# Performance work log

Hardware: AMD Instinct MI355X
Metric: run time of the kernel (lower is better)

Reference implementation:

```python
import jax, jax.numpy as jnp
import numpy as np

B, L, D, H, DFF, WS = 8, 16384, 256, 8, 1024, 32
HD = D // H
NW = L // WS


def setup_inputs() -> dict:
    key = jax.random.key(0)
    ks = jax.random.split(key, 12)
    p = lambda k, sh: jax.random.normal(k, sh, jnp.float32) * 0.02
    return {
        "query_em": jax.random.normal(ks[0], (B, L, D), jnp.float32),
        "key_value_em": jax.random.normal(ks[1], (B, L, D), jnp.float32),
        "Wq": p(ks[2], (D, D)), "bq": jnp.zeros((D,), jnp.float32),
        "Wk": p(ks[3], (D, D)), "bk": jnp.zeros((D,), jnp.float32),
        "Wv": p(ks[4], (D, D)), "bv": jnp.zeros((D,), jnp.float32),
        "Wo": p(ks[5], (D, D)), "bo": jnp.zeros((D,), jnp.float32),
        "g1": jnp.ones((D,), jnp.float32), "be1": jnp.zeros((D,), jnp.float32),
        "W1": p(ks[6], (D, DFF)), "bf1": jnp.zeros((DFF,), jnp.float32),
        "W2": p(ks[7], (DFF, D)), "bf2": jnp.zeros((D,), jnp.float32),
        "g2": jnp.ones((D,), jnp.float32), "be2": jnp.zeros((D,), jnp.float32),
    }


def _layernorm(x, g, b):
    m = jnp.mean(x, axis=-1, keepdims=True)
    v = jnp.var(x, axis=-1, keepdims=True)
    return (x - m) * jax.lax.rsqrt(v + 1e-5) * g + b


def _encoder_layer(q, kv, Wq, bq, Wk, bk, Wv, bv, Wo, bo, g1, be1, W1, bf1, W2, bf2, g2, be2):
    # q, kv: [B, NW, WS, D] -- attention only within each window of WS tokens
    b, nw, ws, d = q.shape
    qh = (q @ Wq + bq).reshape(b, nw, ws, H, HD)
    kh = (kv @ Wk + bk).reshape(b, nw, ws, H, HD)
    vh = (kv @ Wv + bv).reshape(b, nw, ws, H, HD)
    scores = jnp.einsum("bnqhd,bnkhd->bnhqk", qh, kh) / np.sqrt(HD).astype(np.float32)
    attn = jax.nn.softmax(scores, axis=-1)
    o = jnp.einsum("bnhqk,bnkhd->bnqhd", attn, vh).reshape(b, nw, ws, d)
    o = o @ Wo + bo
    x = _layernorm(q + o, g1, be1)  # post-LN residual
    f = jax.nn.relu(x @ W1 + bf1) @ W2 + bf2
    return _layernorm(x + f, g2, be2)


def reference(query_em, key_value_em, Wq, bq, Wk, bk, Wv, bv, Wo, bo,
              g1, be1, W1, bf1, W2, bf2, g2, be2):
    params = (Wq, bq, Wk, bk, Wv, bv, Wo, bo, g1, be1, W1, bf1, W2, bf2, g2, be2)
    q = query_em.reshape(B, NW, WS, D)
    kv = key_value_em.reshape(B, NW, WS, D)
    x = _encoder_layer(q, kv, *params)
    # cyclic shift by half a window-count along the window axis, second pass, shift back
    x = jnp.roll(x, -WS // 2, axis=1)
    x = _encoder_layer(x, x, *params)
    x = jnp.roll(x, WS // 2, axis=1)
    return x.reshape(B, L, D)
```

## Files before the change

### kernel.cpp

```cpp
#include <hip/hip_runtime.h>
#include <cstdint>
#include <cstddef>

typedef unsigned short u16;
typedef __bf16 bf16x8 __attribute__((ext_vector_type(8)));
typedef float f32x4 __attribute__((ext_vector_type(4)));
typedef unsigned short u16x8 __attribute__((ext_vector_type(8)));
typedef unsigned short u16x4 __attribute__((ext_vector_type(4)));

__device__ __forceinline__ u16 f2bf(float f) {
  union { float f; unsigned u; } x; x.f = f;
  unsigned r = x.u + 0x7fffu + ((x.u >> 16) & 1u);
  return (u16)(r >> 16);
}
__device__ __forceinline__ float bf2f(u16 u) {
  union { unsigned u; float f; } x; x.u = ((unsigned)u) << 16;
  return x.f;
}
__device__ __forceinline__ void gload16(const void* g, void* l) {
  __builtin_amdgcn_global_load_lds(
      (const __attribute__((address_space(1))) unsigned int*)g,
      (__attribute__((address_space(3))) unsigned int*)l, 16, 0, 0);
}

template<int MODE, int AF32>
__global__ __launch_bounds__(256) void gemm_bt(
    const void* __restrict__ Ap_, int lda, const u16* __restrict__ Bt,
    const float* __restrict__ bias, u16* __restrict__ C0, int ldc, int coff,
    u16* __restrict__ C2, int vsplit, int N, int K, int gy)
{
  __shared__ u16 As[2][128 * 32];
  __shared__ u16 Bs[2][128 * 32];
  const int tid  = threadIdx.x;
  const int lane = tid & 63, w = tid >> 6;
  const int nwg = gridDim.x, o = blockIdx.x;
  const int lid = (o & 7) * (nwg >> 3) + (o >> 3);
  const int by = lid % gy, bx = lid / gy;
  const int row0 = bx * 128, col0 = by * 128;
  const int wr = (w >> 1) * 64, wc = (w & 1) * 64;
  const int fr = lane & 15, fg = lane >> 4;
  const int srow  = (w << 5) + (lane >> 2);
  const int sslot = (lane & 3) ^ ((lane >> 2) & 3);
  const u16*   Ab = (const u16*)Ap_;
  const float* Af = (const float*)Ap_;

  auto stageB = [&](int buf, int k0) {
    #pragma unroll
    for (int h = 0; h < 2; ++h)
      gload16((const char*)Bt + ((size_t)(col0 + srow + h*16) * K + k0) * 2 + sslot*16,
              &Bs[buf][((w << 5) + h*16) * 32]);
  };
  auto stageA16 = [&](int buf, int k0) {
    #pragma unroll
    for (int h = 0; h < 2; ++h)
      gload16((const char*)Ab + ((size_t)(row0 + srow + h*16) * lda + k0) * 2 + sslot*16,
              &As[buf][((w << 5) + h*16) * 32]);
  };
  f32x4 pre[2][2];
  auto loadA32 = [&](int k0) {
    #pragma unroll
    for (int p = 0; p < 2; ++p) {
      const int sidx = tid + p*256, rr = sidx >> 2, sl = sidx & 3;
      const float* src = &Af[(size_t)(row0 + rr) * lda + k0 + sl*8];
      pre[p][0] = *(const f32x4*)src;
      pre[p][1] = *(const f32x4*)(src + 4);
    }
  };
  auto writeA32 = [&](int buf) {
    #pragma unroll
    for (int p = 0; p < 2; ++p) {
      const int sidx = tid + p*256, rr = sidx >> 2, sl = sidx & 3;
      u16x8 o = { f2bf(pre[p][0][0]), f2bf(pre[p][0][1]),
                  f2bf(pre[p][0][2]), f2bf(pre[p][0][3]),
                  f2bf(pre[p][1][0]), f2bf(pre[p][1][1]),
                  f2bf(pre[p][1][2]), f2bf(pre[p][1][3]) };
      *(u16x8*)&As[buf][rr*32 + ((sl ^ (rr & 3)) << 3)] = o;
    }
  };

  f32x4 acc[4][4] = {};

  if (AF32) { loadA32(0); stageB(0, 0); writeA32(0); }
  else      { stageA16(0, 0); stageB(0, 0); }
  __syncthreads();
  int cur = 0;
  for (int k0 = 0; k0 < K; k0 += 32) {
    const int has_next = (k0 + 32 < K);
    if (has_next) {
      if (AF32) loadA32(k0 + 32);
      else      stageA16(cur ^ 1, k0 + 32);
      stageB(cur ^ 1, k0 + 32);
    }
    bf16x8 af[4], bf[4];
    #pragma unroll
    for (int i = 0; i < 4; ++i) {
      const int r = wr + i*16 + fr;
      af[i] = *(const bf16x8*)&As[cur][r*32 + ((fg ^ (fr & 3)) << 3)];
    }
    #pragma unroll
    for (int j = 0; j < 4; ++j) {
      const int r = wc + j*16 + fr;
      bf[j] = *(const bf16x8*)&Bs[cur][r*32 + ((fg ^ (fr & 3)) << 3)];
    }
    #pragma unroll
    for (int i = 0; i < 4; ++i)
      #pragma unroll
      for (int j = 0; j < 4; ++j)
        acc[i][j] = __builtin_amdgcn_mfma_f32_16x16x32_bf16(af[i], bf[j], acc[i][j], 0, 0, 0);
    if (AF32 && has_next) writeA32(cur ^ 1);
    __syncthreads();
    cur ^= 1;
  }

  const int vpart = (MODE == 3) || (MODE == 2 && col0 >= vsplit);
  #pragma unroll
  for (int j = 0; j < 4; ++j) {
    const int c  = col0 + wc + j*16 + fr;
    const float bv = bias[c];
    #pragma unroll
    for (int i = 0; i < 4; ++i) {
      if (vpart) {
        const int cv = (MODE == 2) ? c - vsplit : c;
        const int rb = row0 + wr + i*16 + fg*4;
        u16x4 vv;
        #pragma unroll
        for (int t = 0; t < 4; ++t) vv[t] = f2bf(acc[i][j][t] + bv);
        *(u16x4*)&C2[((size_t)(rb >> 5) * 256 + cv) * 32 + (rb & 31)] = vv;
      } else {
        #pragma unroll
        for (int t = 0; t < 4; ++t) {
          const int r = row0 + wr + i*16 + fg*4 + t;
          float v = acc[i][j][t] + bv;
          if (MODE == 1) v = v > 0.f ? v : 0.f;
          C0[(size_t)r * ldc + coff + c] = f2bf(v);
        }
      }
    }
  }
}

template<int RES_F32>
__global__ __launch_bounds__(512) void gemm_oln(
    const u16* __restrict__ Ap, int lda, const u16* __restrict__ Bt,
    const float* __restrict__ bias, const void* __restrict__ Res,
    const float* __restrict__ g, const float* __restrict__ be,
    u16* __restrict__ Y, int K)
{
  __shared__ u16 As[2][128 * 32];
  __shared__ u16 Bs[2][256 * 32];
  __shared__ float2 red[128][4];
  __shared__ float2 stats[128];
  const int tid  = threadIdx.x;
  const int lane = tid & 63, w = tid >> 6;
  const int nwg = gridDim.x, o = blockIdx.x;
  const int lid = (o & 7) * (nwg >> 3) + (o >> 3);
  const int row0 = lid * 128;
  const int wr = (w >> 2) * 64, wc = (w & 3) * 64;
  const int fr = lane & 15, fg = lane >> 4;
  const int sr   = lane >> 2;
  const int sslot = (lane & 3) ^ ((lane >> 2) & 3);

  auto stage = [&](int buf, int k0) {
    gload16((const char*)Ap + ((size_t)(row0 + (w << 4) + sr) * lda + k0) * 2 + sslot*16,
            &As[buf][((w << 4)) * 32]);
    #pragma unroll
    for (int h = 0; h < 2; ++h)
      gload16((const char*)Bt + ((size_t)((w << 5) + h*16 + sr) * K + k0) * 2 + sslot*16,
              &Bs[buf][((w << 5) + h*16) * 32]);
  };

  f32x4 acc[4][4] = {};

  stage(0, 0);
  __syncthreads();
  int cur = 0;
  for (int k0 = 0; k0 < K; k0 += 32) {
    if (k0 + 32 < K) stage(cur ^ 1, k0 + 32);
    bf16x8 af[4], bf[4];
    #pragma unroll
    for (int i = 0; i < 4; ++i) {
      const int r = wr + i*16 + fr;
      af[i] = *(const bf16x8*)&As[cur][r*32 + ((fg ^ (fr & 3)) << 3)];
    }
    #pragma unroll
    for (int j = 0; j < 4; ++j) {
      const int r = wc + j*16 + fr;
      bf[j] = *(const bf16x8*)&Bs[cur][r*32 + ((fg ^ (fr & 3)) << 3)];
    }
    #pragma unroll
    for (int i = 0; i < 4; ++i)
      #pragma unroll
      for (int j = 0; j < 4; ++j)
        acc[i][j] = __builtin_amdgcn_mfma_f32_16x16x32_bf16(af[i], bf[j], acc[i][j], 0, 0, 0);
    __syncthreads();
    cur ^= 1;
  }

  float ps[4][4] = {}, pq[4][4] = {};
  #pragma unroll
  for (int j = 0; j < 4; ++j) {
    const int c = wc + j*16 + fr;
    const float bv = bias[c];
    #pragma unroll
    for (int i = 0; i < 4; ++i) {
      #pragma unroll
      for (int t = 0; t < 4; ++t) {
        const int r = row0 + wr + i*16 + fg*4 + t;
        const float rv = RES_F32 ? ((const float*)Res)[(size_t)r * 256 + c]
                                 : bf2f(((const u16*)Res)[(size_t)r * 256 + c]);
        float v = acc[i][j][t] + bv + rv;
        acc[i][j][t] = v;
        ps[i][t] += v;
        pq[i][t] += v * v;
      }
    }
  }
  #pragma unroll
  for (int d = 1; d < 16; d <<= 1) {
    #pragma unroll
    for (int i = 0; i < 4; ++i)
      #pragma unroll
      for (int t = 0; t < 4; ++t) {
        ps[i][t] += __shfl_xor(ps[i][t], d, 64);
        pq[i][t] += __shfl_xor(pq[i][t], d, 64);
      }
  }
  if (fr == 0) {
    #pragma unroll
    for (int i = 0; i < 4; ++i)
      #pragma unroll
      for (int t = 0; t < 4; ++t)
        red[wr + i*16 + fg*4 + t][w & 3] = make_float2(ps[i][t], pq[i][t]);
  }
  __syncthreads();
  if (tid < 128) {
    float S = 0.f, Q = 0.f;
    #pragma unroll
    for (int ww = 0; ww < 4; ++ww) { float2 p = red[tid][ww]; S += p.x; Q += p.y; }
    const float m = S * (1.f/256.f);
    const float var = Q * (1.f/256.f) - m*m;
    stats[tid] = make_float2(m, rsqrtf(var + 1e-5f));
  }
  __syncthreads();
  #pragma unroll
  for (int i = 0; i < 4; ++i) {
    #pragma unroll
    for (int t = 0; t < 4; ++t) {
      const int rl = wr + i*16 + fg*4 + t;
      const float2 st = stats[rl];
      const size_t r = row0 + rl;
      #pragma unroll
      for (int j = 0; j < 4; ++j) {
        const int c = wc + j*16 + fr;
        Y[r * 256 + c] = f2bf((acc[i][j][t] - st.x) * st.y * g[c] + be[c]);
      }
    }
  }
}

template<int OUT_F32>
__global__ __launch_bounds__(512, 2) void ffn_fused(
    const u16* __restrict__ X, const u16* __restrict__ W1T,
    const float* __restrict__ b1, const u16* __restrict__ W2T,
    const float* __restrict__ b2, const float* __restrict__ g,
    const float* __restrict__ be, void* __restrict__ Y)
{
  __shared__ u16 W1s[4][32 * 256];
  __shared__ u16 W2s[4][256 * 32];
  __shared__ u16 Hs[8][32 * 32];
  __shared__ float b1s[1024];
  const int tid = threadIdx.x, lane = tid & 63, w = tid >> 6;
  const int fr = lane & 15, fg = lane >> 4;
  const int row0 = blockIdx.x * 256 + w * 32;
  u16* Hw = &Hs[w][0];
  const int hxor = (fr >> 1) & 3;

  auto stage = [&](int buf, int hb) {
    #pragma unroll
    for (int h = 0; h < 2; ++h) {
      const int r = w*4 + h*2 + (lane >> 5);
      const int sl = (lane & 31) ^ (r & 7);
      gload16((const char*)W1T + ((size_t)((hb << 5) + r) * 256 + sl*8) * 2,
              &W1s[buf][(w*4 + h*2) * 256]);
    }
    #pragma unroll
    for (int h = 0; h < 2; ++h) {
      const int r = w*32 + h*16 + (lane >> 2);
      const int sl = (lane & 3) ^ ((r >> 1) & 3);
      gload16((const char*)W2T + ((size_t)r * 1024 + (hb << 5) + sl*8) * 2,
              &W2s[buf][(w*32 + h*16) * 32]);
    }
  };

  if (tid < 256) {
    f32x4 bv = *(const f32x4*)&b1[tid * 4];
    *(f32x4*)&b1s[tid * 4] = bv;
  }
  bf16x8 af[2][8];
  #pragma unroll
  for (int g2 = 0; g2 < 2; ++g2)
    #pragma unroll
    for (int kf = 0; kf < 8; ++kf)
      af[g2][kf] = *(const bf16x8*)&X[(size_t)(row0 + g2*16 + fr) * 256 + kf*32 + fg*8];
  asm volatile("s_waitcnt vmcnt(0)" ::: "memory");

  f32x4 acc2[2][16] = {};

  auto compute_slice = [&](int hb, int cur) {
    f32x4 acc1[2][2] = {};
    #pragma unroll
    for (int kf = 0; kf < 8; ++kf) {
      #pragma unroll
      for (int hf = 0; hf < 2; ++hf) {
        const int n = hf*16 + fr;
        bf16x8 w1f = *(const bf16x8*)&W1s[cur][n*256 + ((((kf << 2) | fg) ^ (n & 7)) << 3)];
        acc1[hf][0] = __builtin_amdgcn_mfma_f32_16x16x32_bf16(w1f, af[0][kf], acc1[hf][0], 0, 0, 0);
        acc1[hf][1] = __builtin_amdgcn_mfma_f32_16x16x32_bf16(w1f, af[1][kf], acc1[hf][1], 0, 0, 0);
      }
    }
    #pragma unroll
    for (int g2 = 0; g2 < 2; ++g2) {
      #pragma unroll
      for (int hf = 0; hf < 2; ++hf) {
        const int h0 = hf*16 + fg*4;
        f32x4 b4 = *(const f32x4*)&b1s[(hb << 5) + h0];
        u16x4 hv;
        #pragma unroll
        for (int t = 0; t < 4; ++t) {
          float v = acc1[hf][g2][t] + b4[t];
          hv[t] = f2bf(v > 0.f ? v : 0.f);
        }
        const int tok = g2*16 + fr;
        *(u16x4*)((char*)Hw + tok*64 + ((((hf << 1) | (fg >> 1)) ^ hxor) << 4)
                                     + ((fg & 1) << 3)) = hv;
      }
    }
    asm volatile("s_waitcnt lgkmcnt(0)" ::: "memory");
    __builtin_amdgcn_sched_barrier(0);

    bf16x8 hf2[2];
    #pragma unroll
    for (int g2 = 0; g2 < 2; ++g2) {
      const int tok = g2*16 + fr;
      hf2[g2] = *(const bf16x8*)((char*)Hw + tok*64 + ((fg ^ hxor) << 4));
    }
    #pragma unroll
    for (int nf = 0; nf < 16; ++nf) {
      const int n = nf*16 + fr;
      bf16x8 w2f = *(const bf16x8*)&W2s[cur][n*32 + ((fg ^ ((n >> 1) & 3)) << 3)];
      acc2[0][nf] = __builtin_amdgcn_mfma_f32_16x16x32_bf16(hf2[0], w2f, acc2[0][nf], 0, 0, 0);
      acc2[1][nf] = __builtin_amdgcn_mfma_f32_16x16x32_bf16(hf2[1], w2f, acc2[1][nf], 0, 0, 0);
    }
  };

  stage(0, 0);
  stage(1, 1);
  for (int hb = 0; hb < 30; ++hb) {
    stage((hb + 2) & 3, hb + 2);
    asm volatile("s_waitcnt vmcnt(8)" ::: "memory");
    __builtin_amdgcn_s_barrier();
    __builtin_amdgcn_sched_barrier(0);
    compute_slice(hb, hb & 3);
  }
  asm volatile("s_waitcnt vmcnt(4)" ::: "memory");
  __builtin_amdgcn_s_barrier();
  __builtin_amdgcn_sched_barrier(0);
  compute_slice(30, 30 & 3);
  asm volatile("s_waitcnt vmcnt(0)" ::: "memory");
  __builtin_amdgcn_s_barrier();
  __builtin_amdgcn_sched_barrier(0);
  compute_slice(31, 31 & 3);

  #pragma unroll
  for (int g2 = 0; g2 < 2; ++g2) {
    const int rbase = row0 + g2*16 + fg*4;
    float s1[4] = {}, sq[4] = {};
    #pragma unroll
    for (int nf = 0; nf < 16; ++nf) {
      const int c = nf*16 + fr;
      const float b = b2[c];
      #pragma unroll
      for (int t = 0; t < 4; ++t) {
        float v = acc2[g2][nf][t] + b + bf2f(X[(size_t)(rbase + t) * 256 + c]);
        acc2[g2][nf][t] = v;
        s1[t] += v; sq[t] += v * v;
      }
    }
    #pragma unroll
    for (int d = 1; d < 16; d <<= 1) {
      #pragma unroll
      for (int t = 0; t < 4; ++t) {
        s1[t] += __shfl_xor(s1[t], d, 64);
        sq[t] += __shfl_xor(sq[t], d, 64);
      }
    }
    float mean[4], rstd[4];
    #pragma unroll
    for (int t = 0; t < 4; ++t) {
      mean[t] = s1[t] * (1.f/256.f);
      const float var = sq[t] * (1.f/256.f) - mean[t]*mean[t];
      rstd[t] = rsqrtf(var + 1e-5f);
    }
    #pragma unroll
    for (int nf = 0; nf < 16; ++nf) {
      const int c = nf*16 + fr;
      const float gc = g[c], bc = be[c];
      #pragma unroll
      for (int t = 0; t < 4; ++t) {
        const float y = (acc2[g2][nf][t] - mean[t]) * rstd[t] * gc + bc;
        if (OUT_F32) ((float*)Y)[(size_t)(rbase + t) * 256 + c] = y;
        else         ((u16*)Y)[(size_t)(rbase + t) * 256 + c] = f2bf(y);
      }
    }
  }
}

__global__ __launch_bounds__(256) void attn_mfma(
    const u16* Q, int sq, const u16* __restrict__ K, int sk,
    const u16* __restrict__ Vt, u16* O, int so)
{
  __shared__ u16 P[4][32 * 40];
  const int tid = threadIdx.x, lane = tid & 63, w = tid >> 6;
  const int win = blockIdx.x * 4 + w;
  const size_t q0 = (size_t)win * 32;
  const int fr = lane & 15, fg = lane >> 4;
  u16* Pw = &P[w][0];
  const float scale = 0.17677669529663687f;

  for (int h = 0; h < 8; ++h) {
    const int co = h * 32;
    bf16x8 qa[2], kb[2];
    #pragma unroll
    for (int i = 0; i < 2; ++i)
      qa[i] = *(const bf16x8*)&Q[(q0 + i*16 + fr) * sq + co + fg*8];
    #pragma unroll
    for (int j = 0; j < 2; ++j)
      kb[j] = *(const bf16x8*)&K[(q0 + j*16 + fr) * sk + co + fg*8];
    f32x4 s[2][2] = {};
    #pragma unroll
    for (int i = 0; i < 2; ++i)
      #pragma unroll
      for (int j = 0; j < 2; ++j)
        s[i][j] = __builtin_amdgcn_mfma_f32_16x16x32_bf16(qa[i], kb[j], s[i][j], 0, 0, 0);

    float inv[2][4];
    #pragma unroll
    for (int i = 0; i < 2; ++i) {
      #pragma unroll
      for (int t = 0; t < 4; ++t) {
        float a0 = s[i][0][t] * scale, a1 = s[i][1][t] * scale;
        float mx = fmaxf(a0, a1);
        #pragma unroll
        for (int d = 1; d < 16; d <<= 1) mx = fmaxf(mx, __shfl_xor(mx, d, 64));
        const float p0 = __expf(a0 - mx), p1 = __expf(a1 - mx);
        float sm = p0 + p1;
        #pragma unroll
        for (int d = 1; d < 16; d <<= 1) sm += __shfl_xor(sm, d, 64);
        inv[i][t] = 1.f / sm;
        const int q = i*16 + fg*4 + t;
        Pw[q*40 + fr]      = f2bf(p0);
        Pw[q*40 + 16 + fr] = f2bf(p1);
      }
    }

    bf16x8 pa[2], vb[2];
    #pragma unroll
    for (int i = 0; i < 2; ++i)
      pa[i] = *(const bf16x8*)&Pw[(i*16 + fr)*40 + fg*8];
    #pragma unroll
    for (int j = 0; j < 2; ++j)
      vb[j] = *(const bf16x8*)&Vt[(size_t)win*8192 + (co + j*16 + fr)*32 + fg*8];
    f32x4 oacc[2][2] = {};
    #pragma unroll
    for (int i = 0; i < 2; ++i)
      #pragma unroll
      for (int j = 0; j < 2; ++j)
        oacc[i][j] = __builtin_amdgcn_mfma_f32_16x16x32_bf16(pa[i], vb[j], oacc[i][j], 0, 0, 0);

    #pragma unroll
    for (int i = 0; i < 2; ++i)
      #pragma unroll
      for (int j = 0; j < 2; ++j)
        #pragma unroll
        for (int t = 0; t < 4; ++t)
          O[(q0 + i*16 + fg*4 + t) * so + co + j*16 + fr] =
              f2bf(oacc[i][j][t] * inv[i][t]);
  }
}

__global__ __launch_bounds__(256) void wprep(
    const float* __restrict__ W, u16* __restrict__ Wt, int K, int N)
{
  const int idx = blockIdx.x * 256 + threadIdx.x;
  if (idx >= K * N) return;
  const int k = idx / N, n = idx - k * N;
  Wt[(size_t)n * K + k] = f2bf(W[idx]);
}

__global__ __launch_bounds__(256) void bcat(
    const float* __restrict__ a, const float* __restrict__ b,
    const float* __restrict__ c, float* __restrict__ o)
{
  const int i = blockIdx.x * 256 + threadIdx.x;
  o[i] = i < 256 ? a[i] : (i < 512 ? b[i - 256] : c[i - 512]);
}

extern "C" void kernel_launch(void* const* d_in, const int* in_sizes, int n_in,
                              void* d_out, int out_size, void* d_ws, size_t ws_size,
                              hipStream_t stream)
{
  const float* query  = (const float*)d_in[0];
  const float* keyval = (const float*)d_in[1];
  const float* Wq = (const float*)d_in[2];  const float* bq  = (const float*)d_in[3];
  const float* Wk = (const float*)d_in[4];  const float* bk  = (const float*)d_in[5];
  const float* Wv = (const float*)d_in[6];  const float* bv  = (const float*)d_in[7];
  const float* Wo = (const float*)d_in[8];  const float* bo  = (const float*)d_in[9];
  const float* g1 = (const float*)d_in[10]; const float* be1 = (const float*)d_in[11];
  const float* W1 = (const float*)d_in[12]; const float* bf1 = (const float*)d_in[13];
  const float* W2 = (const float*)d_in[14]; const float* bf2 = (const float*)d_in[15];
  const float* g2 = (const float*)d_in[16]; const float* be2 = (const float*)d_in[17];

  const int M = 131072;
  char* ws = (char*)d_ws;
  u16*  xcur = (u16*)ws;
  u16*  x1   = (u16*)(ws + (64ull  << 20));
  u16*  QKc  = (u16*)(ws + (256ull << 20));
  u16*  Vtc  = (u16*)(ws + (384ull << 20));
  u16*  WqkvT = (u16*)(ws + (448ull << 20));
  u16*  WoT   = WqkvT + 196608;
  u16*  W1T   = WoT   + 65536;
  u16*  W2T   = W1T   + 262144;
  float* bqkv = (float*)(W2T + 262144);
  float* bkv  = bqkv + 256;

  wprep<<<256,  256, 0, stream>>>(Wq, WqkvT,          256, 256);
  wprep<<<256,  256, 0, stream>>>(Wk, WqkvT +  65536, 256, 256);
  wprep<<<256,  256, 0, stream>>>(Wv, WqkvT + 131072, 256, 256);
  wprep<<<256,  256, 0, stream>>>(Wo, WoT, 256, 256);
  wprep<<<1024, 256, 0, stream>>>(W1, W1T, 256, 1024);
  wprep<<<1024, 256, 0, stream>>>(W2, W2T, 1024, 256);
  bcat<<<3, 256, 0, stream>>>(bq, bk, bv, bqkv);


  gemm_bt<0,1><<<2048, 256, 0, stream>>>(
      query, 256, WqkvT, bq, QKc, 512, 0, nullptr, 0, 256, 256, 2);
  gemm_bt<2,1><<<4096, 256, 0, stream>>>(
      keyval, 256, WqkvT + 65536, bkv, QKc, 512, 256, Vtc, 256, 512, 256, 4);
  attn_mfma<<<1024, 256, 0, stream>>>(QKc, 512, QKc + 256, 512, Vtc, QKc, 512);
  gemm_oln<1><<<1024, 512, 0, stream>>>(
      QKc, 512, WoT, bo, query, g1, be1, x1, 256);
  ffn_fused<0><<<512, 512, 0, stream>>>(
      x1, W1T, bf1, W2T, bf2, g2, be2, xcur);

  gemm_bt<2,0><<<6144, 256, 0, stream>>>(
      xcur, 256, WqkvT, bqkv, QKc, 512, 0, Vtc, 512, 768, 256, 6);
  attn_mfma<<<1024, 256, 0, stream>>>(QKc, 512, QKc + 256, 512, Vtc, QKc, 512);
  gemm_oln<0><<<1024, 512, 0, stream>>>(
      QKc, 512, WoT, bo, xcur, g1, be1, x1, 256);
  ffn_fused<1><<<512, 512, 0, stream>>>(
      x1, W1T, bf1, W2T, bf2, g2, be2, d_out);
}
```

Measured before the change: 895.8 us.

## Software-pipeline FFN GEMM1 and GEMM2 across slices with double-buffered hidden tile

Splits the per-slice FFN work into gemm1 (W1 plus bias plus ReLU into LDS) and gemm2 (H times W2), and skews them so gemm1 of slice t runs alongside gemm2 of slice t-1. The hidden-activation LDS buffer is double-buffered, and W1 staging drops to three buffers to make room. This removes the lgkmcnt wait between writing H and reading it back, and the loop barrier moves before the stage issue. It also raises wave priority with s_setprio during the MFMA sections. In exchange the pipeline gets more complex and the tail needs careful buffer-reuse ordering; W1 at three buffers with a prefetch distance of two leaves little margin.

```diff
diff --git a/kernel.cpp b/kernel.cpp
--- a/kernel.cpp
+++ b/kernel.cpp
@@ -265,30 +265,30 @@
     const float* __restrict__ b2, const float* __restrict__ g,
     const float* __restrict__ be, void* __restrict__ Y)
 {
-  __shared__ u16 W1s[4][32 * 256];
+  __shared__ u16 W1s[3][32 * 256];
   __shared__ u16 W2s[4][256 * 32];
-  __shared__ u16 Hs[8][32 * 32];
+  __shared__ u16 Hs[2][8][32 * 32];
   __shared__ float b1s[1024];
   const int tid = threadIdx.x, lane = tid & 63, w = tid >> 6;
   const int fr = lane & 15, fg = lane >> 4;
   const int row0 = blockIdx.x * 256 + w * 32;
-  u16* Hw = &Hs[w][0];
   const int hxor = (fr >> 1) & 3;
 
-  auto stage = [&](int buf, int hb) {
+  auto stage = [&](int t) {
+    const int b1f = t % 3, b2f = t & 3;
     #pragma unroll
     for (int h = 0; h < 2; ++h) {
       const int r = w*4 + h*2 + (lane >> 5);
       const int sl = (lane & 31) ^ (r & 7);
-      gload16((const char*)W1T + ((size_t)((hb << 5) + r) * 256 + sl*8) * 2,
-              &W1s[buf][(w*4 + h*2) * 256]);
+      gload16((const char*)W1T + ((size_t)((t << 5) + r) * 256 + sl*8) * 2,
+              &W1s[b1f][(w*4 + h*2) * 256]);
     }
     #pragma unroll
     for (int h = 0; h < 2; ++h) {
       const int r = w*32 + h*16 + (lane >> 2);
       const int sl = (lane & 3) ^ ((r >> 1) & 3);
-      gload16((const char*)W2T + ((size_t)r * 1024 + (hb << 5) + sl*8) * 2,
-              &W2s[buf][(w*32 + h*16) * 32]);
+      gload16((const char*)W2T + ((size_t)r * 1024 + (t << 5) + sl*8) * 2,
+              &W2s[b2f][(w*32 + h*16) * 32]);
     }
   };
 
@@ -302,11 +302,13 @@
     #pragma unroll
     for (int kf = 0; kf < 8; ++kf)
       af[g2][kf] = *(const bf16x8*)&X[(size_t)(row0 + g2*16 + fr) * 256 + kf*32 + fg*8];
-  asm volatile("s_waitcnt vmcnt(0)" ::: "memory");
+  asm volatile("s_waitcnt vmcnt(0) lgkmcnt(0)" ::: "memory");
 
   f32x4 acc2[2][16] = {};
 
-  auto compute_slice = [&](int hb, int cur) {
+  auto gemm1 = [&](int t) {
+    const int cur = t % 3;
+    u16* Hw = &Hs[t & 1][w][0];
     f32x4 acc1[2][2] = {};
     #pragma unroll
     for (int kf = 0; kf < 8; ++kf) {
@@ -323,26 +325,27 @@
       #pragma unroll
       for (int hf = 0; hf < 2; ++hf) {
         const int h0 = hf*16 + fg*4;
-        f32x4 b4 = *(const f32x4*)&b1s[(hb << 5) + h0];
+        f32x4 b4 = *(const f32x4*)&b1s[(t << 5) + h0];
         u16x4 hv;
         #pragma unroll
-        for (int t = 0; t < 4; ++t) {
-          float v = acc1[hf][g2][t] + b4[t];
-          hv[t] = f2bf(v > 0.f ? v : 0.f);
+        for (int tt = 0; tt < 4; ++tt) {
+          float v = acc1[hf][g2][tt] + b4[tt];
+          hv[tt] = f2bf(v > 0.f ? v : 0.f);
         }
         const int tok = g2*16 + fr;
         *(u16x4*)((char*)Hw + tok*64 + ((((hf << 1) | (fg >> 1)) ^ hxor) << 4)
                                      + ((fg & 1) << 3)) = hv;
       }
     }
-    asm volatile("s_waitcnt lgkmcnt(0)" ::: "memory");
-    __builtin_amdgcn_sched_barrier(0);
-
+  };
+  auto gemm2 = [&](int t) {
+    const int cur = t & 3;
+    const u16* Hw = &Hs[t & 1][w][0];
     bf16x8 hf2[2];
     #pragma unroll
     for (int g2 = 0; g2 < 2; ++g2) {
       const int tok = g2*16 + fr;
-      hf2[g2] = *(const bf16x8*)((char*)Hw + tok*64 + ((fg ^ hxor) << 4));
+      hf2[g2] = *(const bf16x8*)((const char*)Hw + tok*64 + ((fg ^ hxor) << 4));
     }
     #pragma unroll
     for (int nf = 0; nf < 16; ++nf) {
@@ -353,23 +356,28 @@
     }
   };
 
-  stage(0, 0);
-  stage(1, 1);
-  for (int hb = 0; hb < 30; ++hb) {
-    stage((hb + 2) & 3, hb + 2);
+  stage(0);
+  stage(1);
+  for (int t = 0; t < 30; ++t) {
+    __builtin_amdgcn_s_barrier();
+    stage(t + 2);
     asm volatile("s_waitcnt vmcnt(8)" ::: "memory");
-    __builtin_amdgcn_s_barrier();
-    __builtin_amdgcn_sched_barrier(0);
-    compute_slice(hb, hb & 3);
-  }
+    __builtin_amdgcn_s_setprio(1);
+    gemm1(t);
+    if (t > 0) gemm2(t - 1);
+    __builtin_amdgcn_s_setprio(0);
+  }
+  __builtin_amdgcn_s_barrier();
   asm volatile("s_waitcnt vmcnt(4)" ::: "memory");
+  __builtin_amdgcn_s_setprio(1);
+  gemm1(30); gemm2(29);
+  __builtin_amdgcn_s_setprio(0);
   __builtin_amdgcn_s_barrier();
-  __builtin_amdgcn_sched_barrier(0);
-  compute_slice(30, 30 & 3);
   asm volatile("s_waitcnt vmcnt(0)" ::: "memory");
-  __builtin_amdgcn_s_barrier();
-  __builtin_amdgcn_sched_barrier(0);
-  compute_slice(31, 31 & 3);
+  __builtin_amdgcn_s_setprio(1);
+  gemm1(31); gemm2(30);
+  gemm2(31);
+  __builtin_amdgcn_s_setprio(0);
 
   #pragma unroll
   for (int g2 = 0; g2 < 2; ++g2) {
```

Result: slower. 937.1 us (+4.6%).
